# Optimization experiments

Measured on AMD Instinct MI355X. Metric: run time of the kernel, lower is better.

## Reference

```python
import jax, jax.numpy as jnp
import numpy as np

# 3D PGA grade slices over the 16-component multivector (contiguous in standard basis order)
GRADE_SLICES = [(0, 1), (1, 5), (5, 11), (11, 15), (15, 16)]
GRADE_DIMS = [1, 4, 6, 4, 1]


def setup_inputs() -> dict:
    key = jax.random.key(0)
    ks = jax.random.split(key, 11)
    x = jax.random.normal(ks[0], (8, 2048, 128, 16), dtype=jnp.float32)
    inp = {"x": x}
    for g, d in enumerate(GRADE_DIMS):
        # match nn.Linear default init scale ~ U(-1/sqrt(d), 1/sqrt(d)); randn is fine for a numeric baseline
        inp[f"w{g}"] = jax.random.normal(ks[1 + 2 * g], (d, d), dtype=jnp.float32) / np.sqrt(d)
        inp[f"b{g}"] = jax.random.normal(ks[2 + 2 * g], (d,), dtype=jnp.float32) / np.sqrt(d)
    return inp


def reference(x, w0, b0, w1, b1, w2, b2, w3, b3, w4, b4):
    ws = [w0, w1, w2, w3, w4]
    bs = [b0, b1, b2, b3, b4]
    # Block-diagonal per-grade linear: gather slice, y = x_g @ W_g^T + b_g, scatter back.
    # Since grade index sets are contiguous, scatter == concatenate along last dim.
    outs = []
    for (lo, hi), w, b in zip(GRADE_SLICES, ws, bs):
        xg = x[..., lo:hi]                       # [..., d_g]
        outs.append(jnp.einsum("...i,oi->...o", xg, w) + b)
    return jnp.concatenate(outs, axis=-1)        # [..., 16]
```

## Files before the change

kernel.cpp:

```cpp
#include <hip/hip_runtime.h>


typedef float v4f __attribute__((ext_vector_type(4)));

__global__ __launch_bounds__(256) void GradeWiseLinear_kernel(
    const float* __restrict__ x,
    const float* __restrict__ w0, const float* __restrict__ b0,
    const float* __restrict__ w1, const float* __restrict__ b1,
    const float* __restrict__ w2, const float* __restrict__ b2,
    const float* __restrict__ w3, const float* __restrict__ b3,
    const float* __restrict__ w4, const float* __restrict__ b4,
    float* __restrict__ out, int n4)
{
    __shared__ float s[86];
    {
        int t = threadIdx.x;
        if (t < 86) {
            float v;
            if      (t == 0)  v = w0[0];
            else if (t < 17)  v = w1[t - 1];
            else if (t < 53)  v = w2[t - 17];
            else if (t < 69)  v = w3[t - 53];
            else if (t == 69) v = w4[0];
            else if (t == 70) v = b0[0];
            else if (t < 75)  v = b1[t - 71];
            else if (t < 81)  v = b2[t - 75];
            else if (t < 85)  v = b3[t - 81];
            else              v = b4[0];
            s[t] = v;
        }
    }
    __syncthreads();

    const int t = threadIdx.x;
    const int base = blockIdx.x * 1024 + t;
    const int j = t & 3;

    const v4f* xv = (const v4f*)x;

    v4f me[4];
    #pragma unroll
    for (int k = 0; k < 4; ++k) me[k] = xv[base + 256 * k];

    float up_y[4], up_z[4], up_w[4], dn_x[4], dn_y[4], dn_z[4];
    #pragma unroll
    for (int k = 0; k < 4; ++k) {
        up_y[k] = __shfl_up(me[k].y, 1);
        up_z[k] = __shfl_up(me[k].z, 1);
        up_w[k] = __shfl_up(me[k].w, 1);
        dn_x[k] = __shfl_down(me[k].x, 1);
        dn_y[k] = __shfl_down(me[k].y, 1);
        dn_z[k] = __shfl_down(me[k].z, 1);
    }

    v4f r[4];

    if (j == 0) {
        #pragma unroll
        for (int k = 0; k < 4; ++k) {
            r[k].x = s[70] + me[k].x * s[0];
            r[k].y = s[71] + me[k].y * s[1] + me[k].z * s[2]  + me[k].w * s[3]  + dn_x[k] * s[4];
            r[k].z = s[72] + me[k].y * s[5] + me[k].z * s[6]  + me[k].w * s[7]  + dn_x[k] * s[8];
            r[k].w = s[73] + me[k].y * s[9] + me[k].z * s[10] + me[k].w * s[11] + dn_x[k] * s[12];
        }
    } else if (j == 1) {
        #pragma unroll
        for (int k = 0; k < 4; ++k) {
            r[k].x = s[74] + up_y[k] * s[13] + up_z[k] * s[14] + up_w[k] * s[15] + me[k].x * s[16];
            r[k].y = s[75] + me[k].y * s[17] + me[k].z * s[18] + me[k].w * s[19]
                           + dn_x[k] * s[20] + dn_y[k] * s[21] + dn_z[k] * s[22];
            r[k].z = s[76] + me[k].y * s[23] + me[k].z * s[24] + me[k].w * s[25]
                           + dn_x[k] * s[26] + dn_y[k] * s[27] + dn_z[k] * s[28];
            r[k].w = s[77] + me[k].y * s[29] + me[k].z * s[30] + me[k].w * s[31]
                           + dn_x[k] * s[32] + dn_y[k] * s[33] + dn_z[k] * s[34];
        }
    } else if (j == 2) {
        #pragma unroll
        for (int k = 0; k < 4; ++k) {
            r[k].x = s[78] + up_y[k] * s[35] + up_z[k] * s[36] + up_w[k] * s[37]
                           + me[k].x * s[38] + me[k].y * s[39] + me[k].z * s[40];
            r[k].y = s[79] + up_y[k] * s[41] + up_z[k] * s[42] + up_w[k] * s[43]
                           + me[k].x * s[44] + me[k].y * s[45] + me[k].z * s[46];
            r[k].z = s[80] + up_y[k] * s[47] + up_z[k] * s[48] + up_w[k] * s[49]
                           + me[k].x * s[50] + me[k].y * s[51] + me[k].z * s[52];
            r[k].w = s[81] + me[k].w * s[53] + dn_x[k] * s[54] + dn_y[k] * s[55] + dn_z[k] * s[56];
        }
    } else {
        #pragma unroll
        for (int k = 0; k < 4; ++k) {
            r[k].x = s[82] + up_w[k] * s[57] + me[k].x * s[58] + me[k].y * s[59] + me[k].z * s[60];
            r[k].y = s[83] + up_w[k] * s[61] + me[k].x * s[62] + me[k].y * s[63] + me[k].z * s[64];
            r[k].z = s[84] + up_w[k] * s[65] + me[k].x * s[66] + me[k].y * s[67] + me[k].z * s[68];
            r[k].w = s[85] + me[k].w * s[69];
        }
    }

    v4f* ov = (v4f*)out;
    #pragma unroll
    for (int k = 0; k < 4; ++k)
        __builtin_nontemporal_store(r[k], ov + base + 256 * k);
}

extern "C" void kernel_launch(void* const* d_in, const int* in_sizes, int n_in,
                              void* d_out, int out_size, void* d_ws, size_t ws_size,
                              hipStream_t stream) {
    const float* x  = (const float*)d_in[0];
    const float* w0 = (const float*)d_in[1];
    const float* b0 = (const float*)d_in[2];
    const float* w1 = (const float*)d_in[3];
    const float* b1 = (const float*)d_in[4];
    const float* w2 = (const float*)d_in[5];
    const float* b2 = (const float*)d_in[6];
    const float* w3 = (const float*)d_in[7];
    const float* b3 = (const float*)d_in[8];
    const float* w4 = (const float*)d_in[9];
    const float* b4 = (const float*)d_in[10];
    float* out = (float*)d_out;

    int n4 = in_sizes[0] / 4;
    int block = 256;
    int grid = n4 / (block * 4);

    GradeWiseLinear_kernel<<<grid, block, 0, stream>>>(
        x, w0, b0, w1, b1, w2, b2, w3, b3, w4, b4, out, n4);
}
```

Before: 248.1 us.

## Use persistent grid-stride blocks with software-prefetched next tile

Replaces one-tile-per-block launch with a fixed grid of 1024 persistent blocks that loop over tiles in grid-stride order. Each iteration issues loads for the next tile before computing and storing the current one, overlapping memory latency with compute. This amortizes the per-block shared-memory weight setup, at the cost of more registers per thread and reduced parallelism from the fixed grid size.

```diff
diff --git a/kernel.cpp b/kernel.cpp
--- a/kernel.cpp
+++ b/kernel.cpp
@@ -10,7 +10,7 @@
     const float* __restrict__ w2, const float* __restrict__ b2,
     const float* __restrict__ w3, const float* __restrict__ b3,
     const float* __restrict__ w4, const float* __restrict__ b4,
-    float* __restrict__ out, int n4)
+    float* __restrict__ out, int n_tiles)
 {
     __shared__ float s[86];
     {
@@ -33,72 +33,89 @@
     __syncthreads();
 
     const int t = threadIdx.x;
-    const int base = blockIdx.x * 1024 + t;
     const int j = t & 3;
+    const v4f* xv = (const v4f*)x;
+    v4f* ov = (v4f*)out;
 
-    const v4f* xv = (const v4f*)x;
+    int tt = blockIdx.x;
+    int base = tt * 1024 + t;
 
-    v4f me[4];
+    v4f cur[4];
     #pragma unroll
-    for (int k = 0; k < 4; ++k) me[k] = xv[base + 256 * k];
+    for (int k = 0; k < 4; ++k) cur[k] = xv[base + 256 * k];
 
-    float up_y[4], up_z[4], up_w[4], dn_x[4], dn_y[4], dn_z[4];
-    #pragma unroll
-    for (int k = 0; k < 4; ++k) {
-        up_y[k] = __shfl_up(me[k].y, 1);
-        up_z[k] = __shfl_up(me[k].z, 1);
-        up_w[k] = __shfl_up(me[k].w, 1);
-        dn_x[k] = __shfl_down(me[k].x, 1);
-        dn_y[k] = __shfl_down(me[k].y, 1);
-        dn_z[k] = __shfl_down(me[k].z, 1);
-    }
+    while (true) {
+        const int tt_n = tt + (int)gridDim.x;
+        const bool have_next = tt_n < n_tiles;
+        const int base_n = tt_n * 1024 + t;
+        v4f nxt[4];
+        if (have_next) {
+            #pragma unroll
+            for (int k = 0; k < 4; ++k) nxt[k] = xv[base_n + 256 * k];
+        }
 
-    v4f r[4];
-
-    if (j == 0) {
+        float up_y[4], up_z[4], up_w[4], dn_x[4], dn_y[4], dn_z[4];
         #pragma unroll
         for (int k = 0; k < 4; ++k) {
-            r[k].x = s[70] + me[k].x * s[0];
-            r[k].y = s[71] + me[k].y * s[1] + me[k].z * s[2]  + me[k].w * s[3]  + dn_x[k] * s[4];
-            r[k].z = s[72] + me[k].y * s[5] + me[k].z * s[6]  + me[k].w * s[7]  + dn_x[k] * s[8];
-            r[k].w = s[73] + me[k].y * s[9] + me[k].z * s[10] + me[k].w * s[11] + dn_x[k] * s[12];
+            up_y[k] = __shfl_up(cur[k].y, 1);
+            up_z[k] = __shfl_up(cur[k].z, 1);
+            up_w[k] = __shfl_up(cur[k].w, 1);
+            dn_x[k] = __shfl_down(cur[k].x, 1);
+            dn_y[k] = __shfl_down(cur[k].y, 1);
+            dn_z[k] = __shfl_down(cur[k].z, 1);
         }
-    } else if (j == 1) {
+
+        v4f r[4];
+        if (j == 0) {
+            #pragma unroll
+            for (int k = 0; k < 4; ++k) {
+                r[k].x = s[70] + cur[k].x * s[0];
+                r[k].y = s[71] + cur[k].y * s[1] + cur[k].z * s[2]  + cur[k].w * s[3]  + dn_x[k] * s[4];
+                r[k].z = s[72] + cur[k].y * s[5] + cur[k].z * s[6]  + cur[k].w * s[7]  + dn_x[k] * s[8];
+                r[k].w = s[73] + cur[k].y * s[9] + cur[k].z * s[10] + cur[k].w * s[11] + dn_x[k] * s[12];
+            }
+        } else if (j == 1) {
+            #pragma unroll
+            for (int k = 0; k < 4; ++k) {
+                r[k].x = s[74] + up_y[k] * s[13] + up_z[k] * s[14] + up_w[k] * s[15] + cur[k].x * s[16];
+                r[k].y = s[75] + cur[k].y * s[17] + cur[k].z * s[18] + cur[k].w * s[19]
+                               + dn_x[k] * s[20] + dn_y[k] * s[21] + dn_z[k] * s[22];
+                r[k].z = s[76] + cur[k].y * s[23] + cur[k].z * s[24] + cur[k].w * s[25]
+                               + dn_x[k] * s[26] + dn_y[k] * s[27] + dn_z[k] * s[28];
+                r[k].w = s[77] + cur[k].y * s[29] + cur[k].z * s[30] + cur[k].w * s[31]
+                               + dn_x[k] * s[32] + dn_y[k] * s[33] + dn_z[k] * s[34];
+            }
+        } else if (j == 2) {
+            #pragma unroll
+            for (int k = 0; k < 4; ++k) {
+                r[k].x = s[78] + up_y[k] * s[35] + up_z[k] * s[36] + up_w[k] * s[37]
+                               + cur[k].x * s[38] + cur[k].y * s[39] + cur[k].z * s[40];
+                r[k].y = s[79] + up_y[k] * s[41] + up_z[k] * s[42] + up_w[k] * s[43]
+                               + cur[k].x * s[44] + cur[k].y * s[45] + cur[k].z * s[46];
+                r[k].z = s[80] + up_y[k] * s[47] + up_z[k] * s[48] + up_w[k] * s[49]
+                               + cur[k].x * s[50] + cur[k].y * s[51] + cur[k].z * s[52];
+                r[k].w = s[81] + cur[k].w * s[53] + dn_x[k] * s[54] + dn_y[k] * s[55] + dn_z[k] * s[56];
+            }
+        } else {
+            #pragma unroll
+            for (int k = 0; k < 4; ++k) {
+                r[k].x = s[82] + up_w[k] * s[57] + cur[k].x * s[58] + cur[k].y * s[59] + cur[k].z * s[60];
+                r[k].y = s[83] + up_w[k] * s[61] + cur[k].x * s[62] + cur[k].y * s[63] + cur[k].z * s[64];
+                r[k].z = s[84] + up_w[k] * s[65] + cur[k].x * s[66] + cur[k].y * s[67] + cur[k].z * s[68];
+                r[k].w = s[85] + cur[k].w * s[69];
+            }
+        }
+
         #pragma unroll
-        for (int k = 0; k < 4; ++k) {
-            r[k].x = s[74] + up_y[k] * s[13] + up_z[k] * s[14] + up_w[k] * s[15] + me[k].x * s[16];
-            r[k].y = s[75] + me[k].y * s[17] + me[k].z * s[18] + me[k].w * s[19]
-                           + dn_x[k] * s[20] + dn_y[k] * s[21] + dn_z[k] * s[22];
-            r[k].z = s[76] + me[k].y * s[23] + me[k].z * s[24] + me[k].w * s[25]
-                           + dn_x[k] * s[26] + dn_y[k] * s[27] + dn_z[k] * s[28];
-            r[k].w = s[77] + me[k].y * s[29] + me[k].z * s[30] + me[k].w * s[31]
-                           + dn_x[k] * s[32] + dn_y[k] * s[33] + dn_z[k] * s[34];
-        }
-    } else if (j == 2) {
+        for (int k = 0; k < 4; ++k)
+            __builtin_nontemporal_store(r[k], ov + base + 256 * k);
+
+        if (!have_next) break;
         #pragma unroll
-        for (int k = 0; k < 4; ++k) {
-            r[k].x = s[78] + up_y[k] * s[35] + up_z[k] * s[36] + up_w[k] * s[37]
-                           + me[k].x * s[38] + me[k].y * s[39] + me[k].z * s[40];
-            r[k].y = s[79] + up_y[k] * s[41] + up_z[k] * s[42] + up_w[k] * s[43]
-                           + me[k].x * s[44] + me[k].y * s[45] + me[k].z * s[46];
-            r[k].z = s[80] + up_y[k] * s[47] + up_z[k] * s[48] + up_w[k] * s[49]
-                           + me[k].x * s[50] + me[k].y * s[51] + me[k].z * s[52];
-            r[k].w = s[81] + me[k].w * s[53] + dn_x[k] * s[54] + dn_y[k] * s[55] + dn_z[k] * s[56];
-        }
-    } else {
-        #pragma unroll
-        for (int k = 0; k < 4; ++k) {
-            r[k].x = s[82] + up_w[k] * s[57] + me[k].x * s[58] + me[k].y * s[59] + me[k].z * s[60];
-            r[k].y = s[83] + up_w[k] * s[61] + me[k].x * s[62] + me[k].y * s[63] + me[k].z * s[64];
-            r[k].z = s[84] + up_w[k] * s[65] + me[k].x * s[66] + me[k].y * s[67] + me[k].z * s[68];
-            r[k].w = s[85] + me[k].w * s[69];
-        }
+        for (int k = 0; k < 4; ++k) cur[k] = nxt[k];
+        tt = tt_n;
+        base = base_n;
     }
-
-    v4f* ov = (v4f*)out;
-    #pragma unroll
-    for (int k = 0; k < 4; ++k)
-        __builtin_nontemporal_store(r[k], ov + base + 256 * k);
 }
 
 extern "C" void kernel_launch(void* const* d_in, const int* in_sizes, int n_in,
@@ -118,9 +135,10 @@
     float* out = (float*)d_out;
 
     int n4 = in_sizes[0] / 4;
+    int n_tiles = n4 / 1024;
     int block = 256;
-    int grid = n4 / (block * 4);
+    int grid = 1024;
 
     GradeWiseLinear_kernel<<<grid, block, 0, stream>>>(
-        x, w0, b0, w1, b1, w2, b2, w3, b3, w4, b4, out, n4);
+        x, w0, b0, w1, b1, w2, b2, w3, b3, w4, b4, out, n_tiles);
 }
```

Measured after the change: 249.8 us. No clear change (+0.7%).
